# Kernel tuning notes

Measured on AMD Instinct MI355X. Metric: run time of the kernel, lower is better.

The kernel has to match this reference:

```python
import jax, jax.numpy as jnp
import numpy as np

N = 50000
D = 256
E = 800000


def setup_inputs() -> dict:
    key = jax.random.key(0)
    ks = jax.random.split(key, 8)
    x = jax.random.normal(ks[0], (N, D), dtype=jnp.float32)
    edge_index = jax.random.randint(ks[1], (2, E), 0, N, dtype=jnp.int64)
    s = 1.0 / np.sqrt(D)
    # SAGEConv layer 0 params: lin_l (neighbors, with bias), lin_r (root, no bias)
    Wl0 = jax.random.uniform(ks[2], (D, D), jnp.float32, -s, s)
    bl0 = jnp.zeros((D,), jnp.float32)
    Wr0 = jax.random.uniform(ks[3], (D, D), jnp.float32, -s, s)
    # SAGEConv layer 1 params
    Wl1 = jax.random.uniform(ks[4], (D, D), jnp.float32, -s, s)
    bl1 = jnp.zeros((D,), jnp.float32)
    Wr1 = jax.random.uniform(ks[5], (D, D), jnp.float32, -s, s)
    return {"x": x, "edge_index": edge_index, "Wl0": Wl0, "bl0": bl0, "Wr0": Wr0,
            "Wl1": Wl1, "bl1": bl1, "Wr1": Wr1}


def _sage_conv(x, edge_index, Wl, bl, Wr):
    # PyG SAGEConv, aggr='mean': out = lin_l(mean_{j in N(i)} x_j) + lin_r(x_i)
    src, dst = edge_index[0], edge_index[1]
    msg = x[src]                                            # [E, D] gather
    agg = jax.ops.segment_sum(msg, dst, num_segments=x.shape[0])
    cnt = jax.ops.segment_sum(jnp.ones((edge_index.shape[1],), x.dtype), dst,
                              num_segments=x.shape[0])
    mean = agg / jnp.maximum(cnt, 1.0)[:, None]             # zero-degree -> 0
    return mean @ Wl + bl + x @ Wr


def reference(x, edge_index, Wl0, bl0, Wr0, Wl1, bl1, Wr1):
    negative_slope = 0.5
    target = x  # full-graph path: target nodes = all nodes
    h = x
    # dropout p=0.0 -> identity
    h = _sage_conv(h, edge_index, Wl0, bl0, Wr0)
    h = jnp.where(h >= 0, h, negative_slope * h)
    h = _sage_conv(h, edge_index, Wl1, bl1, Wr1)
    h = jnp.where(h >= 0, h, negative_slope * h)
    return (h, target)
```

## Files before the change

### kernel.cpp

```cpp
#include <hip/hip_runtime.h>
#include <hip/hip_fp8.h>


typedef __attribute__((ext_vector_type(8))) short bf16x8;
typedef __attribute__((ext_vector_type(4))) float f32x4;

__device__ __forceinline__ float bf2f(unsigned short b) {
    union { unsigned u; float f; } x; x.u = ((unsigned)b) << 16; return x.f;
}
__device__ __forceinline__ short f2bf(float f) {
    union { float f; unsigned u; } x; x.f = f;
    unsigned r = x.u + 0x7fffu + ((x.u >> 16) & 1u);
    return (short)(r >> 16);
}
__device__ __forceinline__ unsigned char f2fp8(float f) {
    __hip_fp8_e4m3 q(f);
    return (unsigned char)q.__x;
}
__device__ __forceinline__ float fp82f(unsigned char b) {
    __hip_fp8_e4m3 q; q.__x = (__hip_fp8_storage_t)b;
    return (float)q;
}


__global__ __launch_bounds__(256) void zero_kernel(int* __restrict__ p, int n4) {
    int i = blockIdx.x * 256 + threadIdx.x;
    if (i < n4) *reinterpret_cast<int4*>(p + i * 4) = (int4){0, 0, 0, 0};
}

#define BINA_CHUNK 8192
__global__ __launch_bounds__(512) void bkcount_kernel(
    const int* __restrict__ ei, int* __restrict__ bkcnt, int E, int NBK) {
    __shared__ int hist[512];
    int base_e = blockIdx.x * BINA_CHUNK;
    int nloc = E - base_e;
    if (nloc > BINA_CHUNK) nloc = BINA_CHUNK;
    for (int b = threadIdx.x; b < NBK; b += 512) hist[b] = 0;
    __syncthreads();
    for (int t = threadIdx.x; t < nloc; t += 512)
        atomicAdd(&hist[ei[E + base_e + t] >> 7], 1);
    __syncthreads();
    for (int b = threadIdx.x; b < NBK; b += 512) {
        int h = hist[b];
        if (h > 0) atomicAdd(&bkcnt[b], h);
    }
}

__global__ __launch_bounds__(512) void bkscan_kernel(
    const int* __restrict__ bkcnt, int* __restrict__ bkoff,
    int* __restrict__ bcur, int* __restrict__ offs, int NBK, int N, int E) {
    __shared__ int sm[512];
    int tid = threadIdx.x;
    int v = (tid < NBK) ? bkcnt[tid] : 0;
    sm[tid] = v;
    __syncthreads();
    for (int off = 1; off < 512; off <<= 1) {
        int t = (tid >= off) ? sm[tid - off] : 0;
        __syncthreads();
        sm[tid] += t;
        __syncthreads();
    }
    if (tid < NBK) {
        int e = sm[tid] - v;
        bkoff[tid] = e;
        bcur[tid] = e;
    }
    if (tid == 0) {
        bkoff[NBK] = E;
        offs[N] = E;
    }
}

__global__ __launch_bounds__(512) void binA_kernel(
    const int* __restrict__ ei, int* __restrict__ bcur,
    long long* __restrict__ pairs, int E, int NBK) {
    __shared__ int hist[512];
    int base_e = blockIdx.x * BINA_CHUNK;
    int nloc = E - base_e;
    if (nloc > BINA_CHUNK) nloc = BINA_CHUNK;
    for (int b = threadIdx.x; b < NBK; b += 512) hist[b] = 0;
    __syncthreads();
    for (int t = threadIdx.x; t < nloc; t += 512)
        atomicAdd(&hist[ei[E + base_e + t] >> 7], 1);
    __syncthreads();
    for (int b = threadIdx.x; b < NBK; b += 512) {
        int h = hist[b];
        hist[b] = (h > 0) ? atomicAdd(&bcur[b], h) : 0;
    }
    __syncthreads();
    for (int t = threadIdx.x; t < nloc; t += 512) {
        int dst = ei[E + base_e + t];
        int src = ei[base_e + t];
        int pos = atomicAdd(&hist[dst >> 7], 1);
        pairs[pos] = ((long long)dst << 32) | (unsigned)src;
    }
}

__global__ __launch_bounds__(256) void binB_kernel(
    const long long* __restrict__ pairs, const int* __restrict__ bkoff,
    int* __restrict__ offs, float* __restrict__ invdeg,
    int* __restrict__ csr, int NBK, int N) {
    __shared__ int cnt[128];
    __shared__ int cur[128];
    int b = blockIdx.x;
    int t = threadIdx.x;
    if (t < 128) cnt[t] = 0;
    __syncthreads();
    int beg = bkoff[b];
    int end = bkoff[b + 1];
    for (int i = beg + t; i < end; i += 256)
        atomicAdd(&cnt[((int)(pairs[i] >> 32)) & 127], 1);
    __syncthreads();
    if (t < 64) {
        int c0 = cnt[2 * t], c1 = cnt[2 * t + 1];
        int s = c0 + c1;
        int incl = s;
        #pragma unroll
        for (int d = 1; d < 64; d <<= 1) {
            int x = __shfl_up(incl, d, 64);
            if (t >= d) incl += x;
        }
        int excl = incl - s;
        cur[2 * t] = beg + excl;
        cur[2 * t + 1] = beg + excl + c0;
    }
    __syncthreads();
    if (t < 128) {
        int node = (b << 7) + t;
        if (node < N) {
            offs[node] = cur[t];
            invdeg[node] = 1.0f / (float)(cnt[t] > 0 ? cnt[t] : 1);
        }
    }
    __syncthreads();
    for (int i = beg + t; i < end; i += 256) {
        long long p = pairs[i];
        int pos = atomicAdd(&cur[((int)(p >> 32)) & 127], 1);
        csr[pos] = (int)(p & 0xffffffffLL);
    }
}


__global__ __launch_bounds__(256) void prep_kernel(
    const float* __restrict__ x, short* __restrict__ xb,
    unsigned char* __restrict__ xq, float* __restrict__ xcopy,
    const float* __restrict__ Wl0, const float* __restrict__ Wr0,
    const float* __restrict__ Wl1, const float* __restrict__ Wr1,
    short* __restrict__ B1T, short* __restrict__ B2T, int total8) {
    int gid = blockIdx.x * 256 + threadIdx.x;
    if (gid < total8) {
        const float* p = x + (size_t)gid * 8;
        float4 v0 = *reinterpret_cast<const float4*>(p);
        float4 v1 = *reinterpret_cast<const float4*>(p + 4);
        bf16x8 t;
        t[0] = f2bf(v0.x); t[1] = f2bf(v0.y); t[2] = f2bf(v0.z); t[3] = f2bf(v0.w);
        t[4] = f2bf(v1.x); t[5] = f2bf(v1.y); t[6] = f2bf(v1.z); t[7] = f2bf(v1.w);
        *reinterpret_cast<bf16x8*>(xb + (size_t)gid * 8) = t;
        uchar4 q0, q1;
        q0.x = f2fp8(v0.x); q0.y = f2fp8(v0.y); q0.z = f2fp8(v0.z); q0.w = f2fp8(v0.w);
        q1.x = f2fp8(v1.x); q1.y = f2fp8(v1.y); q1.z = f2fp8(v1.z); q1.w = f2fp8(v1.w);
        *reinterpret_cast<uchar4*>(xq + (size_t)gid * 8) = q0;
        *reinterpret_cast<uchar4*>(xq + (size_t)gid * 8 + 4) = q1;
        *reinterpret_cast<float4*>(xcopy + (size_t)gid * 8) = v0;
        *reinterpret_cast<float4*>(xcopy + (size_t)gid * 8 + 4) = v1;
    } else {
        int idx = gid - total8;
        if (idx < 262144) {
            int sel = idx >> 17;
            int j = idx & 131071;
            int n = j >> 9;
            int k = j & 511;
            const float* Wl = sel ? Wl1 : Wl0;
            const float* Wr = sel ? Wr1 : Wr0;
            float v = (k < 256) ? Wl[k * 256 + n] : Wr[(k - 256) * 256 + n];
            (sel ? B2T : B1T)[j] = f2bf(v);
        }
    }
}

__global__ __launch_bounds__(256) void agg_kernel(
    const unsigned char* __restrict__ feat,
    const int* __restrict__ offs, const int* __restrict__ csr,
    const float* __restrict__ invdeg,
    short* __restrict__ outp, int N) {
    int wave = threadIdx.x >> 6;
    int lane = threadIdx.x & 63;
    int node = blockIdx.x * 4 + wave;
    if (node >= N) return;
    int beg = offs[node];
    int end = offs[node + 1];
    int c = lane * 4;

    float a[4][4];
    #pragma unroll
    for (int u = 0; u < 4; ++u)
        #pragma unroll
        for (int k = 0; k < 4; ++k) a[u][k] = 0.f;

    int deg = end - beg;
    int n8 = deg & ~7;
    for (int t = 0; t < n8; t += 8) {
        int s0 = csr[beg + t];     int s1 = csr[beg + t + 1];
        int s2 = csr[beg + t + 2]; int s3 = csr[beg + t + 3];
        int s4 = csr[beg + t + 4]; int s5 = csr[beg + t + 5];
        int s6 = csr[beg + t + 6]; int s7 = csr[beg + t + 7];
        unsigned u0 = *reinterpret_cast<const unsigned*>(feat + (size_t)s0 * 256 + c);
        unsigned u1 = *reinterpret_cast<const unsigned*>(feat + (size_t)s1 * 256 + c);
        unsigned u2 = *reinterpret_cast<const unsigned*>(feat + (size_t)s2 * 256 + c);
        unsigned u3 = *reinterpret_cast<const unsigned*>(feat + (size_t)s3 * 256 + c);
        unsigned u4 = *reinterpret_cast<const unsigned*>(feat + (size_t)s4 * 256 + c);
        unsigned u5 = *reinterpret_cast<const unsigned*>(feat + (size_t)s5 * 256 + c);
        unsigned u6 = *reinterpret_cast<const unsigned*>(feat + (size_t)s6 * 256 + c);
        unsigned u7 = *reinterpret_cast<const unsigned*>(feat + (size_t)s7 * 256 + c);
        #pragma unroll
        for (int k = 0; k < 4; ++k) a[0][k] += fp82f((u0 >> (8 * k)) & 0xff);
        #pragma unroll
        for (int k = 0; k < 4; ++k) a[1][k] += fp82f((u1 >> (8 * k)) & 0xff);
        #pragma unroll
        for (int k = 0; k < 4; ++k) a[2][k] += fp82f((u2 >> (8 * k)) & 0xff);
        #pragma unroll
        for (int k = 0; k < 4; ++k) a[3][k] += fp82f((u3 >> (8 * k)) & 0xff);
        #pragma unroll
        for (int k = 0; k < 4; ++k) a[0][k] += fp82f((u4 >> (8 * k)) & 0xff);
        #pragma unroll
        for (int k = 0; k < 4; ++k) a[1][k] += fp82f((u5 >> (8 * k)) & 0xff);
        #pragma unroll
        for (int k = 0; k < 4; ++k) a[2][k] += fp82f((u6 >> (8 * k)) & 0xff);
        #pragma unroll
        for (int k = 0; k < 4; ++k) a[3][k] += fp82f((u7 >> (8 * k)) & 0xff);
    }
    for (int e = beg + n8; e < end; ++e) {
        int s = csr[e];
        unsigned u = *reinterpret_cast<const unsigned*>(feat + (size_t)s * 256 + c);
        #pragma unroll
        for (int k = 0; k < 4; ++k) a[0][k] += fp82f((u >> (8 * k)) & 0xff);
    }
    float inv = invdeg[node];
    short4 o;
    o.x = f2bf((a[0][0] + a[1][0] + a[2][0] + a[3][0]) * inv);
    o.y = f2bf((a[0][1] + a[1][1] + a[2][1] + a[3][1]) * inv);
    o.z = f2bf((a[0][2] + a[1][2] + a[2][2] + a[3][2]) * inv);
    o.w = f2bf((a[0][3] + a[1][3] + a[2][3] + a[3][3]) * inv);
    *reinterpret_cast<short4*>(&outp[(size_t)node * 256 + c]) = o;
}

template <int OUT_MODE>
__global__ __launch_bounds__(1024, 4) void gemm_kernel(
    const short* __restrict__ AL, const short* __restrict__ AR,
    const short* __restrict__ BT, const float* __restrict__ bias,
    void* __restrict__ Cout, unsigned char* __restrict__ Cq,
    int M, int ntiles) {
    __shared__ short ldsA[2][32 * 512];
    int wave = threadIdx.x >> 6;
    int lane = threadIdx.x & 63;
    int l16 = lane & 15;
    int lhi = lane >> 4;
    int c0 = wave * 16;

    bf16x8 breg[16];
    #pragma unroll
    for (int kk = 0; kk < 16; ++kk)
        breg[kk] = *reinterpret_cast<const bf16x8*>(
            &BT[(size_t)(c0 + l16) * 512 + kk * 32 + lhi * 8]);
    float bc = bias[c0 + l16];

    auto STAGE = [&](int tt, int buf) {
        #pragma unroll
        for (int i = 0; i < 2; ++i) {
            int r = i * 16 + wave;
            int grow = tt * 32 + r;
            if (grow >= M) grow = M - 1;
            int csw = (lane * 8) ^ ((r & 15) << 3);
            const short* src = (csw < 256)
                ? AL + (size_t)grow * 256 + csw
                : AR + (size_t)grow * 256 + (csw - 256);
            __builtin_amdgcn_global_load_lds(
                (const __attribute__((address_space(1))) unsigned int*)src,
                (__attribute__((address_space(3))) unsigned int*)
                    &ldsA[buf][r * 512],
                16, 0, 0);
        }
    };

    int t = blockIdx.x;
    int stride = gridDim.x;
    if (t >= ntiles) return;
    STAGE(t, 0);
    int buf = 0;
    int it = 0;
    for (; t < ntiles; t += stride, ++it) {
        int tn = t + stride;
        bool havenext = (tn < ntiles);
        if (havenext) STAGE(tn, buf ^ 1);

        if (it == 0) {
            if (havenext) asm volatile("s_waitcnt vmcnt(2)" ::: "memory");
            else          asm volatile("s_waitcnt vmcnt(0)" ::: "memory");
        } else if (havenext) {
            if constexpr (OUT_MODE == 0)
                asm volatile("s_waitcnt vmcnt(18)" ::: "memory");
            else
                asm volatile("s_waitcnt vmcnt(10)" ::: "memory");
        } else {
            if constexpr (OUT_MODE == 0)
                asm volatile("s_waitcnt vmcnt(16)" ::: "memory");
            else
                asm volatile("s_waitcnt vmcnt(8)" ::: "memory");
        }
        __builtin_amdgcn_s_barrier();
        __builtin_amdgcn_sched_barrier(0);

        int row0 = t * 32;
        f32x4 acc[2];
        acc[0] = (f32x4){0.f, 0.f, 0.f, 0.f};
        acc[1] = (f32x4){0.f, 0.f, 0.f, 0.f};

        const short* lb = &ldsA[buf][0];
        #pragma unroll
        for (int kk = 0; kk < 16; ++kk) {
            bf16x8 a0, a1;
            {
                int r = l16;
                int ks = (kk * 32 + lhi * 8) ^ ((r & 15) << 3);
                a0 = *reinterpret_cast<const bf16x8*>(&lb[r * 512 + ks]);
            }
            {
                int r = 16 + l16;
                int ks = (kk * 32 + lhi * 8) ^ ((r & 15) << 3);
                a1 = *reinterpret_cast<const bf16x8*>(&lb[r * 512 + ks]);
            }
            acc[0] = __builtin_amdgcn_mfma_f32_16x16x32_bf16(
                a0, breg[kk], acc[0], 0, 0, 0);
            acc[1] = __builtin_amdgcn_mfma_f32_16x16x32_bf16(
                a1, breg[kk], acc[1], 0, 0, 0);
        }

        #pragma unroll
        for (int mt = 0; mt < 2; ++mt) {
            #pragma unroll
            for (int r = 0; r < 4; ++r) {
                int grow = row0 + mt * 16 + lhi * 4 + r;
                if (grow >= M) grow = M - 1;
                int gcol = c0 + l16;
                float v = acc[mt][r] + bc;
                v = (v >= 0.f) ? v : 0.5f * v;
                if (OUT_MODE == 0) {
                    ((short*)Cout)[(size_t)grow * 256 + gcol] = f2bf(v);
                    Cq[(size_t)grow * 256 + gcol] = f2fp8(v);
                } else {
                    ((float*)Cout)[(size_t)grow * 256 + gcol] = v;
                }
            }
        }
        __builtin_amdgcn_s_barrier();
        buf ^= 1;
    }
}


extern "C" void kernel_launch(void* const* d_in, const int* in_sizes, int n_in,
                              void* d_out, int out_size, void* d_ws, size_t ws_size,
                              hipStream_t stream) {
    const float* x   = (const float*)d_in[0];
    const int*   ei  = (const int*)d_in[1];
    const float* Wl0 = (const float*)d_in[2];
    const float* bl0 = (const float*)d_in[3];
    const float* Wr0 = (const float*)d_in[4];
    const float* Wl1 = (const float*)d_in[5];
    const float* bl1 = (const float*)d_in[6];
    const float* Wr1 = (const float*)d_in[7];

    const int N = in_sizes[0] / 256;
    const int E = in_sizes[1] / 2;
    const int NBK = (N + 127) / 128;

    char* ws = (char*)d_ws;
    size_t o = 0;
    auto alloc = [&](size_t bytes) {
        size_t p = o;
        o = (o + bytes + 255) & ~(size_t)255;
        return p;
    };
    int*   offs   = (int*)  (ws + alloc((size_t)(N + 1) * 4));
    float* invdeg = (float*)(ws + alloc((size_t)N * 4));
    int*   bkcnt  = (int*)  (ws + alloc(((size_t)NBK + 4) * 4));
    int*   bkoff  = (int*)  (ws + alloc(((size_t)NBK + 1) * 4));
    int*   bcur   = (int*)  (ws + alloc((size_t)NBK * 4));
    long long* pairs = (long long*)(ws + alloc((size_t)E * 8));
    int*   csr    = (int*)  (ws + alloc((size_t)E * 4));
    short* xb     = (short*)(ws + alloc((size_t)N * 256 * 2));
    short* meanb  = (short*)(ws + alloc((size_t)N * 256 * 2));
    short* h0     = (short*)(ws + alloc((size_t)N * 256 * 2));
    unsigned char* xq  = (unsigned char*)(ws + alloc((size_t)N * 256));
    unsigned char* h0q = (unsigned char*)(ws + alloc((size_t)N * 256));
    short* B1T    = (short*)(ws + alloc(262144));
    short* B2T    = (short*)(ws + alloc(262144));

    int ebk = (E + BINA_CHUNK - 1) / BINA_CHUNK;
    zero_kernel<<<1, 256, 0, stream>>>(bkcnt, (NBK + 3) / 4);
    bkcount_kernel<<<ebk, 512, 0, stream>>>(ei, bkcnt, E, NBK);
    bkscan_kernel<<<1, 512, 0, stream>>>(bkcnt, bkoff, bcur, offs, NBK, N, E);
    binA_kernel<<<ebk, 512, 0, stream>>>(ei, bcur, pairs, E, NBK);
    binB_kernel<<<NBK, 256, 0, stream>>>(pairs, bkoff, offs, invdeg, csr, NBK, N);

    int total8 = N * 32;
    int prep_threads = total8 + 262144;
    prep_kernel<<<(prep_threads + 255) / 256, 256, 0, stream>>>(
        x, xb, xq, (float*)d_out + (size_t)N * 256,
        Wl0, Wr0, Wl1, Wr1, B1T, B2T, total8);

    int ab = (N + 3) / 4;
    int ntiles = (N + 31) / 32;
    int gblocks = 512;
    agg_kernel<<<ab, 256, 0, stream>>>(xq, offs, csr, invdeg, meanb, N);
    gemm_kernel<0><<<gblocks, 1024, 0, stream>>>(
        meanb, xb, B1T, bl0, h0, h0q, N, ntiles);
    agg_kernel<<<ab, 256, 0, stream>>>(h0q, offs, csr, invdeg, meanb, N);
    gemm_kernel<1><<<gblocks, 1024, 0, stream>>>(
        meanb, h0, B2T, bl1, d_out, nullptr, N, ntiles);
}
```

Measured before the change: 239.4 us.

## Fuse bucket histogram with prep, store per-chunk histograms, drop redundant recount

Measured after the change: 252.2 us. 1.05x slower.

```diff
diff --git a/kernel.cpp b/kernel.cpp
--- a/kernel.cpp
+++ b/kernel.cpp
@@ -22,79 +22,112 @@
     return (float)q;
 }
 
-
-__global__ __launch_bounds__(256) void zero_kernel(int* __restrict__ p, int n4) {
-    int i = blockIdx.x * 256 + threadIdx.x;
-    if (i < n4) *reinterpret_cast<int4*>(p + i * 4) = (int4){0, 0, 0, 0};
-}
-
 #define BINA_CHUNK 8192
-__global__ __launch_bounds__(512) void bkcount_kernel(
-    const int* __restrict__ ei, int* __restrict__ bkcnt, int E, int NBK) {
-    __shared__ int hist[512];
-    int base_e = blockIdx.x * BINA_CHUNK;
+
+
+__global__ __launch_bounds__(512) void bkhist_prep_kernel(
+    const int* __restrict__ ei, int* __restrict__ hist, int E, int NBK, int NCH,
+    const float* __restrict__ x, short* __restrict__ xb,
+    unsigned char* __restrict__ xq, float* __restrict__ xcopy,
+    const float* __restrict__ Wl0, const float* __restrict__ Wr0,
+    const float* __restrict__ Wl1, const float* __restrict__ Wr1,
+    short* __restrict__ B1T, short* __restrict__ B2T, int total8) {
+    if ((int)blockIdx.x < NCH) {
+        __shared__ int h[512];
+        int c = blockIdx.x;
+        int base_e = c * BINA_CHUNK;
+        int nloc = E - base_e;
+        if (nloc > BINA_CHUNK) nloc = BINA_CHUNK;
+        for (int b = threadIdx.x; b < 512; b += 512) h[b] = 0;
+        __syncthreads();
+        for (int t = threadIdx.x; t < nloc; t += 512)
+            atomicAdd(&h[ei[E + base_e + t] >> 7], 1);
+        __syncthreads();
+        if ((int)threadIdx.x < NBK) hist[c * 512 + threadIdx.x] = h[threadIdx.x];
+    } else {
+        int gid = ((int)blockIdx.x - NCH) * 512 + threadIdx.x;
+        if (gid < total8) {
+            const float* p = x + (size_t)gid * 8;
+            float4 v0 = *reinterpret_cast<const float4*>(p);
+            float4 v1 = *reinterpret_cast<const float4*>(p + 4);
+            bf16x8 t;
+            t[0] = f2bf(v0.x); t[1] = f2bf(v0.y); t[2] = f2bf(v0.z); t[3] = f2bf(v0.w);
+            t[4] = f2bf(v1.x); t[5] = f2bf(v1.y); t[6] = f2bf(v1.z); t[7] = f2bf(v1.w);
+            *reinterpret_cast<bf16x8*>(xb + (size_t)gid * 8) = t;
+            uchar4 q0, q1;
+            q0.x = f2fp8(v0.x); q0.y = f2fp8(v0.y); q0.z = f2fp8(v0.z); q0.w = f2fp8(v0.w);
+            q1.x = f2fp8(v1.x); q1.y = f2fp8(v1.y); q1.z = f2fp8(v1.z); q1.w = f2fp8(v1.w);
+            *reinterpret_cast<uchar4*>(xq + (size_t)gid * 8) = q0;
+            *reinterpret_cast<uchar4*>(xq + (size_t)gid * 8 + 4) = q1;
+            *reinterpret_cast<float4*>(xcopy + (size_t)gid * 8) = v0;
+            *reinterpret_cast<float4*>(xcopy + (size_t)gid * 8 + 4) = v1;
+        } else {
+            int idx = gid - total8;
+            if (idx < 262144) {
+                int sel = idx >> 17;
+                int j = idx & 131071;
+                int n = j >> 9;
+                int k = j & 511;
+                const float* Wl = sel ? Wl1 : Wl0;
+                const float* Wr = sel ? Wr1 : Wr0;
+                float v = (k < 256) ? Wl[k * 256 + n] : Wr[(k - 256) * 256 + n];
+                (sel ? B2T : B1T)[j] = f2bf(v);
+            }
+        }
+    }
+}
+
+__global__ __launch_bounds__(512) void bkscan_kernel(
+    int* __restrict__ hist, int* __restrict__ bkoff, int* __restrict__ offs,
+    int NBK, int NCH, int N, int E) {
+    __shared__ int sm[512];
+    int b = threadIdx.x;
+    int run = 0;
+    if (b < NBK) {
+        for (int c = 0; c < NCH; ++c) {
+            int h = hist[c * 512 + b];
+            hist[c * 512 + b] = run;
+            run += h;
+        }
+    }
+    sm[b] = run;
+    __syncthreads();
+    for (int off = 1; off < 512; off <<= 1) {
+        int t = (b >= off) ? sm[b - off] : 0;
+        __syncthreads();
+        sm[b] += t;
+        __syncthreads();
+    }
+    int excl = sm[b] - run;
+    if (b < NBK) {
+        bkoff[b] = excl;
+        for (int c = 0; c < NCH; ++c) hist[c * 512 + b] += excl;
+    }
+    if (b == 0) {
+        bkoff[NBK] = E;
+        offs[N] = E;
+    }
+}
+
+
+__global__ __launch_bounds__(512) void binA_kernel(
+    const int* __restrict__ ei, const int* __restrict__ hist,
+    long long* __restrict__ pairs, int E, int NBK) {
+    __shared__ int pos[512];
+    int c = blockIdx.x;
+    if ((int)threadIdx.x < NBK) pos[threadIdx.x] = hist[c * 512 + threadIdx.x];
+    __syncthreads();
+    int base_e = c * BINA_CHUNK;
     int nloc = E - base_e;
     if (nloc > BINA_CHUNK) nloc = BINA_CHUNK;
-    for (int b = threadIdx.x; b < NBK; b += 512) hist[b] = 0;
-    __syncthreads();
-    for (int t = threadIdx.x; t < nloc; t += 512)
-        atomicAdd(&hist[ei[E + base_e + t] >> 7], 1);
-    __syncthreads();
-    for (int b = threadIdx.x; b < NBK; b += 512) {
-        int h = hist[b];
-        if (h > 0) atomicAdd(&bkcnt[b], h);
-    }
-}
-
-__global__ __launch_bounds__(512) void bkscan_kernel(
-    const int* __restrict__ bkcnt, int* __restrict__ bkoff,
-    int* __restrict__ bcur, int* __restrict__ offs, int NBK, int N, int E) {
-    __shared__ int sm[512];
-    int tid = threadIdx.x;
-    int v = (tid < NBK) ? bkcnt[tid] : 0;
-    sm[tid] = v;
-    __syncthreads();
-    for (int off = 1; off < 512; off <<= 1) {
-        int t = (tid >= off) ? sm[tid - off] : 0;
-        __syncthreads();
-        sm[tid] += t;
-        __syncthreads();
-    }
-    if (tid < NBK) {
-        int e = sm[tid] - v;
-        bkoff[tid] = e;
-        bcur[tid] = e;
-    }
-    if (tid == 0) {
-        bkoff[NBK] = E;
-        offs[N] = E;
-    }
-}
-
-__global__ __launch_bounds__(512) void binA_kernel(
-    const int* __restrict__ ei, int* __restrict__ bcur,
-    long long* __restrict__ pairs, int E, int NBK) {
-    __shared__ int hist[512];
-    int base_e = blockIdx.x * BINA_CHUNK;
-    int nloc = E - base_e;
-    if (nloc > BINA_CHUNK) nloc = BINA_CHUNK;
-    for (int b = threadIdx.x; b < NBK; b += 512) hist[b] = 0;
-    __syncthreads();
-    for (int t = threadIdx.x; t < nloc; t += 512)
-        atomicAdd(&hist[ei[E + base_e + t] >> 7], 1);
-    __syncthreads();
-    for (int b = threadIdx.x; b < NBK; b += 512) {
-        int h = hist[b];
-        hist[b] = (h > 0) ? atomicAdd(&bcur[b], h) : 0;
-    }
-    __syncthreads();
     for (int t = threadIdx.x; t < nloc; t += 512) {
         int dst = ei[E + base_e + t];
         int src = ei[base_e + t];
-        int pos = atomicAdd(&hist[dst >> 7], 1);
-        pairs[pos] = ((long long)dst << 32) | (unsigned)src;
-    }
-}
+        int p = atomicAdd(&pos[dst >> 7], 1);
+        pairs[p] = ((long long)dst << 32) | (unsigned)src;
+    }
+}
+
 
 __global__ __launch_bounds__(256) void binB_kernel(
     const long long* __restrict__ pairs, const int* __restrict__ bkoff,
@@ -137,44 +170,6 @@
         long long p = pairs[i];
         int pos = atomicAdd(&cur[((int)(p >> 32)) & 127], 1);
         csr[pos] = (int)(p & 0xffffffffLL);
-    }
-}
-
-
-__global__ __launch_bounds__(256) void prep_kernel(
-    const float* __restrict__ x, short* __restrict__ xb,
-    unsigned char* __restrict__ xq, float* __restrict__ xcopy,
-    const float* __restrict__ Wl0, const float* __restrict__ Wr0,
-    const float* __restrict__ Wl1, const float* __restrict__ Wr1,
-    short* __restrict__ B1T, short* __restrict__ B2T, int total8) {
-    int gid = blockIdx.x * 256 + threadIdx.x;
-    if (gid < total8) {
-        const float* p = x + (size_t)gid * 8;
-        float4 v0 = *reinterpret_cast<const float4*>(p);
-        float4 v1 = *reinterpret_cast<const float4*>(p + 4);
-        bf16x8 t;
-        t[0] = f2bf(v0.x); t[1] = f2bf(v0.y); t[2] = f2bf(v0.z); t[3] = f2bf(v0.w);
-        t[4] = f2bf(v1.x); t[5] = f2bf(v1.y); t[6] = f2bf(v1.z); t[7] = f2bf(v1.w);
-        *reinterpret_cast<bf16x8*>(xb + (size_t)gid * 8) = t;
-        uchar4 q0, q1;
-        q0.x = f2fp8(v0.x); q0.y = f2fp8(v0.y); q0.z = f2fp8(v0.z); q0.w = f2fp8(v0.w);
-        q1.x = f2fp8(v1.x); q1.y = f2fp8(v1.y); q1.z = f2fp8(v1.z); q1.w = f2fp8(v1.w);
-        *reinterpret_cast<uchar4*>(xq + (size_t)gid * 8) = q0;
-        *reinterpret_cast<uchar4*>(xq + (size_t)gid * 8 + 4) = q1;
-        *reinterpret_cast<float4*>(xcopy + (size_t)gid * 8) = v0;
-        *reinterpret_cast<float4*>(xcopy + (size_t)gid * 8 + 4) = v1;
-    } else {
-        int idx = gid - total8;
-        if (idx < 262144) {
-            int sel = idx >> 17;
-            int j = idx & 131071;
-            int n = j >> 9;
-            int k = j & 511;
-            const float* Wl = sel ? Wl1 : Wl0;
-            const float* Wr = sel ? Wr1 : Wr0;
-            float v = (k < 256) ? Wl[k * 256 + n] : Wr[(k - 256) * 256 + n];
-            (sel ? B2T : B1T)[j] = f2bf(v);
-        }
     }
 }
 
@@ -373,6 +368,7 @@
     const int N = in_sizes[0] / 256;
     const int E = in_sizes[1] / 2;
     const int NBK = (N + 127) / 128;
+    const int NCH = (E + BINA_CHUNK - 1) / BINA_CHUNK;
 
     char* ws = (char*)d_ws;
     size_t o = 0;
@@ -383,9 +379,8 @@
     };
     int*   offs   = (int*)  (ws + alloc((size_t)(N + 1) * 4));
     float* invdeg = (float*)(ws + alloc((size_t)N * 4));
-    int*   bkcnt  = (int*)  (ws + alloc(((size_t)NBK + 4) * 4));
+    int*   hist   = (int*)  (ws + alloc((size_t)NCH * 512 * 4));
     int*   bkoff  = (int*)  (ws + alloc(((size_t)NBK + 1) * 4));
-    int*   bcur   = (int*)  (ws + alloc((size_t)NBK * 4));
     long long* pairs = (long long*)(ws + alloc((size_t)E * 8));
     int*   csr    = (int*)  (ws + alloc((size_t)E * 4));
     short* xb     = (short*)(ws + alloc((size_t)N * 256 * 2));
@@ -396,18 +391,15 @@
     short* B1T    = (short*)(ws + alloc(262144));
     short* B2T    = (short*)(ws + alloc(262144));
 
-    int ebk = (E + BINA_CHUNK - 1) / BINA_CHUNK;
-    zero_kernel<<<1, 256, 0, stream>>>(bkcnt, (NBK + 3) / 4);
-    bkcount_kernel<<<ebk, 512, 0, stream>>>(ei, bkcnt, E, NBK);
-    bkscan_kernel<<<1, 512, 0, stream>>>(bkcnt, bkoff, bcur, offs, NBK, N, E);
-    binA_kernel<<<ebk, 512, 0, stream>>>(ei, bcur, pairs, E, NBK);
-    binB_kernel<<<NBK, 256, 0, stream>>>(pairs, bkoff, offs, invdeg, csr, NBK, N);
-
     int total8 = N * 32;
-    int prep_threads = total8 + 262144;
-    prep_kernel<<<(prep_threads + 255) / 256, 256, 0, stream>>>(
+    int prep_blocks = (total8 + 262144 + 511) / 512;
+    bkhist_prep_kernel<<<NCH + prep_blocks, 512, 0, stream>>>(
+        ei, hist, E, NBK, NCH,
         x, xb, xq, (float*)d_out + (size_t)N * 256,
         Wl0, Wr0, Wl1, Wr1, B1T, B2T, total8);
+    bkscan_kernel<<<1, 512, 0, stream>>>(hist, bkoff, offs, NBK, NCH, N, E);
+    binA_kernel<<<NCH, 512, 0, stream>>>(ei, hist, pairs, E, NBK);
+    binB_kernel<<<NBK, 256, 0, stream>>>(pairs, bkoff, offs, invdeg, csr, NBK, N);
 
     int ab = (N + 3) / 4;
     int ntiles = (N + 31) / 32;
```
